# Performance work log

Measured on AMD Instinct MI355X. Metric: run time of the kernel, lower is better.

## Reference

```python
import jax, jax.numpy as jnp
import numpy as np

NF, B, C, H, W = 5, 8, 64, 128, 128

def setup_inputs() -> dict:
    key = jax.random.key(0)
    k1, k2, k3, k4, k5 = jax.random.split(key, 5)
    return {
        "inp": jax.random.normal(k1, (NF, B, C, H, W), dtype=jnp.float32),
        "origin_w": jax.random.normal(k2, (C, NF * C), dtype=jnp.float32) * 0.05,
        "origin_b": jax.random.normal(k3, (C,), dtype=jnp.float32) * 0.05,
        "out_w": jax.random.normal(k4, (1, 2 * C), dtype=jnp.float32) * 0.05,
        "out_b": jax.random.normal(k5, (1,), dtype=jnp.float32) * 0.05,
    }

def reference(inp, origin_w, origin_b, out_w, out_b):
    nf, b, c, h, w = inp.shape
    # concat frames along channel dim: [b, nf*c, h, w]
    x = jnp.transpose(inp, (1, 0, 2, 3, 4)).reshape(b, nf * c, h, w)
    # 1x1 conv -> origin query, viewed as [b, c, 1, h*w]
    origin = jnp.einsum('ok,bkhw->bohw', origin_w, x) + origin_b[None, :, None, None]
    origin = origin.reshape(b, c, 1, h * w)
    last = inp[-1]  # [b, c, h, w]
    # difference basis: [b, c, nf-1, h*w]
    basis = jnp.stack([last - inp[i] for i in range(nf - 1)], axis=2).reshape(b, c, nf - 1, h * w)
    # L2 normalize over the spatial (last) dim, torch F.normalize semantics (eps=1e-12)
    norm = jnp.sqrt(jnp.sum(basis * basis, axis=-1, keepdims=True))
    basis1 = basis / jnp.maximum(norm, 1e-12)
    # tiny-MN batched matmuls: [b,c,1,hw] x [b,c,hw,nf-1] -> [b,c,1,nf-1]
    score = jnp.einsum('bcik,bcjk->bcij', origin, basis1)
    # [b,c,1,nf-1] x [b,c,nf-1,hw] -> [b,c,1,hw]; original views back as (b,c,w,h)
    out = jnp.einsum('bcij,bcjk->bcik', score, basis1).reshape(b, c, w, h)
    cat = jnp.concatenate([out, last], axis=1)  # [b, 2c, h, w]
    y = jnp.einsum('ok,bkhw->bohw', out_w, cat) + out_b[None, :, None, None]
    return y
```

## Files before the change

### kernel.cpp

```cpp
#include <hip/hip_runtime.h>
#include <math.h>

#define NF 5
#define NB 8
#define NC 64
#define HW 16384
#define NK 320
#define FSTRIDE (NB*NC*HW)

#define EN_FLOATS    (NB*NC*8)

__global__ void k0_wp(const float* __restrict__ W, float* __restrict__ Wp,
                      float* __restrict__ EN){
    const int blk = blockIdx.x, tid = threadIdx.x;
    if (blk == 80){
        float4 z = make_float4(0.f,0.f,0.f,0.f);
#pragma unroll
        for (int j=0; j<4; ++j)
            reinterpret_cast<float4*>(EN)[tid*4 + j] = z;
        return;
    }
    int idx = blk*256 + tid;
    int c = idx / NK;
    int k = idx - c*NK;
    Wp[((c>>2)*NK + k)*4 + (c&3)] = W[idx];
}

__device__ __forceinline__ float redsum64(float v){
#pragma unroll
    for (int m = 1; m < 64; m <<= 1) v += __shfl_xor(v, m, 64);
    return v;
}

__global__ __launch_bounds__(256, 8) void k1_fused(
    const float* __restrict__ inp, const float* __restrict__ Wp,
    const float* __restrict__ bias, float* __restrict__ EN)
{
    const int tid = threadIdx.x;
    const int l   = tid & 63;
    const int wv  = __builtin_amdgcn_readfirstlane(tid >> 6);
    const int blk = blockIdx.x;
    const int xcd  = blk & 7;
    const int slot = blk >> 3;
    const int cgrp = slot & 3;
    const int g    = xcd*64 + (slot >> 2);
    const int b    = g >> 6;
    const int s0   = (g & 63) << 8;
    const int c0   = (cgrp << 4) + (wv << 2);
    const int sl   = __builtin_amdgcn_readfirstlane(c0 >> 2);

    float4 a0,a1,a2,a3;
    {
        float4 bv = *reinterpret_cast<const float4*>(bias + c0);
        a0 = make_float4(bv.x,bv.x,bv.x,bv.x);
        a1 = make_float4(bv.y,bv.y,bv.y,bv.y);
        a2 = make_float4(bv.z,bv.z,bv.z,bv.z);
        a3 = make_float4(bv.w,bv.w,bv.w,bv.w);
    }

    const float* wsl = Wp + (size_t)sl * (NK*4);

#define FMA4(A, WS) \
    A.x = fmaf(WS, xv.x, A.x); A.y = fmaf(WS, xv.y, A.y); \
    A.z = fmaf(WS, xv.z, A.z); A.w = fmaf(WS, xv.w, A.w);

#pragma unroll 1
    for (int f=0; f<NF; ++f){
        const float* xp = inp + (size_t)(f*NB + b)*NC*HW + s0 + (l << 2);
        const float* wf = wsl + f*256;
#pragma unroll 8
        for (int k=0; k<64; ++k){
            float4 xv = *reinterpret_cast<const float4*>(xp);
            xp += HW;
            float4 w  = *reinterpret_cast<const float4*>(wf + (k << 2));
            FMA4(a0, w.x) FMA4(a1, w.y) FMA4(a2, w.z) FMA4(a3, w.w)
        }
    }
#undef FMA4

#define PHASEB(CC, ACC) { \
    const float* cb = inp + ((size_t)b*NC + (c0+(CC)))*HW + s0 + (l << 2); \
    float4 x4 = *reinterpret_cast<const float4*>(cb + (size_t)4*FSTRIDE); \
    float ev[4], nv[4]; \
    _Pragma("unroll") \
    for (int i=0; i<4; ++i){ \
        float4 xi = *reinterpret_cast<const float4*>(cb + (size_t)i*FSTRIDE); \
        float dx = x4.x - xi.x, dy = x4.y - xi.y; \
        float dz = x4.z - xi.z, dw = x4.w - xi.w; \
        nv[i] = fmaf(dx,dx, fmaf(dy,dy, fmaf(dz,dz, dw*dw))); \
        ev[i] = fmaf((ACC).x,dx, fmaf((ACC).y,dy, fmaf((ACC).z,dz, (ACC).w*dw))); \
    } \
    _Pragma("unroll") \
    for (int i=0; i<4; ++i){ ev[i] = redsum64(ev[i]); nv[i] = redsum64(nv[i]); } \
    if (l == 0){ \
        float* p = EN + ((size_t)b*NC + c0 + (CC))*8; \
        atomicAdd(p+0, ev[0]); atomicAdd(p+1, ev[1]); \
        atomicAdd(p+2, ev[2]); atomicAdd(p+3, ev[3]); \
        atomicAdd(p+4, nv[0]); atomicAdd(p+5, nv[1]); \
        atomicAdd(p+6, nv[2]); atomicAdd(p+7, nv[3]); \
    } }

    PHASEB(0, a0) PHASEB(1, a1) PHASEB(2, a2) PHASEB(3, a3)
#undef PHASEB
}

__global__ __launch_bounds__(512) void k3_out(const float* __restrict__ inp,
        const float* __restrict__ EN, const float* __restrict__ out_w,
        const float* __restrict__ out_b, float* __restrict__ y)
{
    __shared__ float  Al[NK];
    __shared__ float4 P[512];
    const int tid = threadIdx.x;
    const int b   = blockIdx.x >> 6;
    const int s0  = (blockIdx.x & 63) << 8;
    const int sg  = tid & 63;
    const int rg  = __builtin_amdgcn_readfirstlane(tid >> 6);

    if (tid < 64){
        const int c = tid;
        const float* e = EN + ((size_t)b*NC + c)*8;
        float w1 = out_w[c], w2 = out_w[NC + c];
        float csum = 0.f;
#pragma unroll
        for (int i=0; i<4; ++i){
            float nc = fmaxf(sqrtf(e[4+i]), 1e-12f);
            float coef = e[i] / (nc*nc);
            Al[i*NC + c] = -w1*coef;
            csum += coef;
        }
        Al[4*NC + c] = w1*csum + w2;
    }
    __syncthreads();

    float4 acc = make_float4(0.f, 0.f, 0.f, 0.f);
    const int rbase = rg*40;
#pragma unroll 8
    for (int j=0; j<40; ++j){
        int r = rbase + j;
        const float* p = inp + (size_t)(((r>>6)*NB + b)*NC + (r&63))*HW + s0 + (sg<<2);
        float  w  = Al[r];
        float4 xv = *reinterpret_cast<const float4*>(p);
        acc.x = fmaf(w, xv.x, acc.x); acc.y = fmaf(w, xv.y, acc.y);
        acc.z = fmaf(w, xv.z, acc.z); acc.w = fmaf(w, xv.w, acc.w);
    }
    P[tid] = acc;
    __syncthreads();
    if (tid < 64){
        float4 r0 = P[tid];
        float vx = r0.x, vy = r0.y, vz = r0.z, vw = r0.w;
#pragma unroll
        for (int gg=1; gg<8; ++gg){
            float4 q = P[tid + (gg<<6)];
            vx += q.x; vy += q.y; vz += q.z; vw += q.w;
        }
        float bb = out_b[0];
        float4 o = make_float4(vx+bb, vy+bb, vz+bb, vw+bb);
        *reinterpret_cast<float4*>(y + (size_t)b*HW + s0 + (tid<<2)) = o;
    }
}

extern "C" void kernel_launch(void* const* d_in, const int* in_sizes, int n_in,
                              void* d_out, int out_size, void* d_ws, size_t ws_size,
                              hipStream_t stream)
{
    const float* inp      = (const float*)d_in[0];
    const float* origin_w = (const float*)d_in[1];
    const float* origin_b = (const float*)d_in[2];
    const float* out_w    = (const float*)d_in[3];
    const float* out_b    = (const float*)d_in[4];
    float* y  = (float*)d_out;
    float* ws = (float*)d_ws;

    float* EN = ws;
    float* Wp = ws + EN_FLOATS;

    k0_wp   <<<81,   256, 0, stream>>>(origin_w, Wp, EN);
    k1_fused<<<2048, 256, 0, stream>>>(inp, Wp, origin_b, EN);
    k3_out  <<<512,  512, 0, stream>>>(inp, EN, out_w, out_b, y);
}
```

Measured before the change: 353.5 us.

## Stage input rows through double-buffered LDS and split output reduction via atomics

The projection kernel now gives each block 1024 spatial positions for 16 output channels. Input rows are staged through a double-buffered shared-memory tile, so every wave reuses the same staged x data across its 4 channels and 4 spatial sub-tiles, with 16 float4 accumulators per thread. The grid drops from 2048 to 512 blocks with occupancy bound 2, trading fewer global re-reads of the input for more registers and lower parallelism. The output kernel splits its 320-row reduction across 8 separate blocks that atomically add into y, which k0 now zeroes, removing the in-block LDS reduction at the cost of float atomics and order-dependent rounding.

```diff
diff --git a/kernel.cpp b/kernel.cpp
--- a/kernel.cpp
+++ b/kernel.cpp
@@ -11,8 +11,15 @@
 #define EN_FLOATS    (NB*NC*8)
 
 __global__ void k0_wp(const float* __restrict__ W, float* __restrict__ Wp,
-                      float* __restrict__ EN){
+                      float* __restrict__ EN, float* __restrict__ y){
     const int blk = blockIdx.x, tid = threadIdx.x;
+    if (blk >= 81){
+        int i = (blk - 81)*256 + tid;
+        float4 z = make_float4(0.f,0.f,0.f,0.f);
+        reinterpret_cast<float4*>(y)[i*2]     = z;
+        reinterpret_cast<float4*>(y)[i*2 + 1] = z;
+        return;
+    }
     if (blk == 80){
         float4 z = make_float4(0.f,0.f,0.f,0.f);
 #pragma unroll
@@ -32,89 +39,143 @@
     return v;
 }
 
-__global__ __launch_bounds__(256, 8) void k1_fused(
+__global__ __launch_bounds__(256, 2) void k1_fused(
     const float* __restrict__ inp, const float* __restrict__ Wp,
     const float* __restrict__ bias, float* __restrict__ EN)
 {
+    __shared__ float S[2*8*1024];
+
     const int tid = threadIdx.x;
     const int l   = tid & 63;
     const int wv  = __builtin_amdgcn_readfirstlane(tid >> 6);
     const int blk = blockIdx.x;
     const int xcd  = blk & 7;
     const int slot = blk >> 3;
+    const int grp  = xcd*16 + (slot >> 2);
     const int cgrp = slot & 3;
-    const int g    = xcd*64 + (slot >> 2);
-    const int b    = g >> 6;
-    const int s0   = (g & 63) << 8;
-    const int c0   = (cgrp << 4) + (wv << 2);
-    const int sl   = __builtin_amdgcn_readfirstlane(c0 >> 2);
-
-    float4 a0,a1,a2,a3;
+    const int b    = grp >> 4;
+    const int s0   = (grp & 15) << 10;
+    const int cf   = (cgrp << 4) + (wv << 2);
+    const int sl   = __builtin_amdgcn_readfirstlane(cgrp*4 + wv);
+
+    float4 a00,a01,a02,a03, a10,a11,a12,a13, a20,a21,a22,a23, a30,a31,a32,a33;
     {
-        float4 bv = *reinterpret_cast<const float4*>(bias + c0);
-        a0 = make_float4(bv.x,bv.x,bv.x,bv.x);
-        a1 = make_float4(bv.y,bv.y,bv.y,bv.y);
-        a2 = make_float4(bv.z,bv.z,bv.z,bv.z);
-        a3 = make_float4(bv.w,bv.w,bv.w,bv.w);
-    }
-
-    const float* wsl = Wp + (size_t)sl * (NK*4);
-
-#define FMA4(A, WS) \
-    A.x = fmaf(WS, xv.x, A.x); A.y = fmaf(WS, xv.y, A.y); \
-    A.z = fmaf(WS, xv.z, A.z); A.w = fmaf(WS, xv.w, A.w);
+        float4 bv = *reinterpret_cast<const float4*>(bias + cf);
+        a00=a01=a02=a03 = make_float4(bv.x,bv.x,bv.x,bv.x);
+        a10=a11=a12=a13 = make_float4(bv.y,bv.y,bv.y,bv.y);
+        a20=a21=a22=a23 = make_float4(bv.z,bv.z,bv.z,bv.z);
+        a30=a31=a32=a33 = make_float4(bv.w,bv.w,bv.w,bv.w);
+    }
+
+    const float* Wk = Wp + (size_t)sl*(NK*4);
+
+#define ROWP(K) (inp + ((size_t)(((K)>>6)*NB + b)*NC + ((K)&63))*HW + s0 + (tid<<2))
+
+    float4 r0,r1,r2,r3,r4,r5,r6,r7;
+#define STAGE_LOAD(KT) { int K0 = (KT)*8; \
+    r0 = *reinterpret_cast<const float4*>(ROWP(K0+0)); \
+    r1 = *reinterpret_cast<const float4*>(ROWP(K0+1)); \
+    r2 = *reinterpret_cast<const float4*>(ROWP(K0+2)); \
+    r3 = *reinterpret_cast<const float4*>(ROWP(K0+3)); \
+    r4 = *reinterpret_cast<const float4*>(ROWP(K0+4)); \
+    r5 = *reinterpret_cast<const float4*>(ROWP(K0+5)); \
+    r6 = *reinterpret_cast<const float4*>(ROWP(K0+6)); \
+    r7 = *reinterpret_cast<const float4*>(ROWP(K0+7)); }
+
+#define STAGE_WRITE(BUF) { float* d = S + (BUF)*8192 + (tid<<2); \
+    *reinterpret_cast<float4*>(d + 0*1024) = r0; \
+    *reinterpret_cast<float4*>(d + 1*1024) = r1; \
+    *reinterpret_cast<float4*>(d + 2*1024) = r2; \
+    *reinterpret_cast<float4*>(d + 3*1024) = r3; \
+    *reinterpret_cast<float4*>(d + 4*1024) = r4; \
+    *reinterpret_cast<float4*>(d + 5*1024) = r5; \
+    *reinterpret_cast<float4*>(d + 6*1024) = r6; \
+    *reinterpret_cast<float4*>(d + 7*1024) = r7; }
+
+#define FMA4(A, WS, XV) \
+    A.x = fmaf(WS, XV.x, A.x); A.y = fmaf(WS, XV.y, A.y); \
+    A.z = fmaf(WS, XV.z, A.z); A.w = fmaf(WS, XV.w, A.w);
+
+    STAGE_LOAD(0)
+    STAGE_WRITE(0)
 
 #pragma unroll 1
-    for (int f=0; f<NF; ++f){
-        const float* xp = inp + (size_t)(f*NB + b)*NC*HW + s0 + (l << 2);
-        const float* wf = wsl + f*256;
-#pragma unroll 8
-        for (int k=0; k<64; ++k){
-            float4 xv = *reinterpret_cast<const float4*>(xp);
-            xp += HW;
-            float4 w  = *reinterpret_cast<const float4*>(wf + (k << 2));
-            FMA4(a0, w.x) FMA4(a1, w.y) FMA4(a2, w.z) FMA4(a3, w.w)
+    for (int kt=0; kt<40; ++kt){
+        __syncthreads();
+        if (kt < 39) STAGE_LOAD(kt+1)
+        const float* X = S + (kt&1)*8192 + (l<<2);
+#pragma unroll 2
+        for (int k=0; k<8; ++k){
+            float4 w  = *reinterpret_cast<const float4*>(Wk + ((kt*8+k)<<2));
+            float4 x0 = *reinterpret_cast<const float4*>(X + k*1024);
+            float4 x1 = *reinterpret_cast<const float4*>(X + k*1024 + 256);
+            float4 x2 = *reinterpret_cast<const float4*>(X + k*1024 + 512);
+            float4 x3 = *reinterpret_cast<const float4*>(X + k*1024 + 768);
+            FMA4(a00,w.x,x0) FMA4(a01,w.x,x1) FMA4(a02,w.x,x2) FMA4(a03,w.x,x3)
+            FMA4(a10,w.y,x0) FMA4(a11,w.y,x1) FMA4(a12,w.y,x2) FMA4(a13,w.y,x3)
+            FMA4(a20,w.z,x0) FMA4(a21,w.z,x1) FMA4(a22,w.z,x2) FMA4(a23,w.z,x3)
+            FMA4(a30,w.w,x0) FMA4(a31,w.w,x1) FMA4(a32,w.w,x2) FMA4(a33,w.w,x3)
         }
+        if (kt < 39) STAGE_WRITE((kt+1)&1)
     }
 #undef FMA4
-
-#define PHASEB(CC, ACC) { \
-    const float* cb = inp + ((size_t)b*NC + (c0+(CC)))*HW + s0 + (l << 2); \
-    float4 x4 = *reinterpret_cast<const float4*>(cb + (size_t)4*FSTRIDE); \
-    float ev[4], nv[4]; \
+#undef STAGE_LOAD
+#undef STAGE_WRITE
+#undef ROWP
+
+#define PHASEB(CH, A0, A1, A2, A3) { \
+    const float* p4 = inp + ((size_t)(4*NB + b)*NC + (cf+(CH)))*HW + s0 + (l<<2); \
+    float4 x40 = *reinterpret_cast<const float4*>(p4); \
+    float4 x41 = *reinterpret_cast<const float4*>(p4 + 256); \
+    float4 x42 = *reinterpret_cast<const float4*>(p4 + 512); \
+    float4 x43 = *reinterpret_cast<const float4*>(p4 + 768); \
     _Pragma("unroll") \
     for (int i=0; i<4; ++i){ \
-        float4 xi = *reinterpret_cast<const float4*>(cb + (size_t)i*FSTRIDE); \
-        float dx = x4.x - xi.x, dy = x4.y - xi.y; \
-        float dz = x4.z - xi.z, dw = x4.w - xi.w; \
-        nv[i] = fmaf(dx,dx, fmaf(dy,dy, fmaf(dz,dz, dw*dw))); \
-        ev[i] = fmaf((ACC).x,dx, fmaf((ACC).y,dy, fmaf((ACC).z,dz, (ACC).w*dw))); \
-    } \
-    _Pragma("unroll") \
-    for (int i=0; i<4; ++i){ ev[i] = redsum64(ev[i]); nv[i] = redsum64(nv[i]); } \
-    if (l == 0){ \
-        float* p = EN + ((size_t)b*NC + c0 + (CC))*8; \
-        atomicAdd(p+0, ev[0]); atomicAdd(p+1, ev[1]); \
-        atomicAdd(p+2, ev[2]); atomicAdd(p+3, ev[3]); \
-        atomicAdd(p+4, nv[0]); atomicAdd(p+5, nv[1]); \
-        atomicAdd(p+6, nv[2]); atomicAdd(p+7, nv[3]); \
+        const float* pi = inp + ((size_t)(i*NB + b)*NC + (cf+(CH)))*HW + s0 + (l<<2); \
+        float4 xi0 = *reinterpret_cast<const float4*>(pi); \
+        float4 xi1 = *reinterpret_cast<const float4*>(pi + 256); \
+        float4 xi2 = *reinterpret_cast<const float4*>(pi + 512); \
+        float4 xi3 = *reinterpret_cast<const float4*>(pi + 768); \
+        float e = 0.f, n = 0.f; \
+        float dx,dy,dz,dw; \
+        dx=x40.x-xi0.x; dy=x40.y-xi0.y; dz=x40.z-xi0.z; dw=x40.w-xi0.w; \
+        n = fmaf(dx,dx, fmaf(dy,dy, fmaf(dz,dz, fmaf(dw,dw, n)))); \
+        e = fmaf(A0.x,dx, fmaf(A0.y,dy, fmaf(A0.z,dz, fmaf(A0.w,dw, e)))); \
+        dx=x41.x-xi1.x; dy=x41.y-xi1.y; dz=x41.z-xi1.z; dw=x41.w-xi1.w; \
+        n = fmaf(dx,dx, fmaf(dy,dy, fmaf(dz,dz, fmaf(dw,dw, n)))); \
+        e = fmaf(A1.x,dx, fmaf(A1.y,dy, fmaf(A1.z,dz, fmaf(A1.w,dw, e)))); \
+        dx=x42.x-xi2.x; dy=x42.y-xi2.y; dz=x42.z-xi2.z; dw=x42.w-xi2.w; \
+        n = fmaf(dx,dx, fmaf(dy,dy, fmaf(dz,dz, fmaf(dw,dw, n)))); \
+        e = fmaf(A2.x,dx, fmaf(A2.y,dy, fmaf(A2.z,dz, fmaf(A2.w,dw, e)))); \
+        dx=x43.x-xi3.x; dy=x43.y-xi3.y; dz=x43.z-xi3.z; dw=x43.w-xi3.w; \
+        n = fmaf(dx,dx, fmaf(dy,dy, fmaf(dz,dz, fmaf(dw,dw, n)))); \
+        e = fmaf(A3.x,dx, fmaf(A3.y,dy, fmaf(A3.z,dz, fmaf(A3.w,dw, e)))); \
+        e = redsum64(e); n = redsum64(n); \
+        if (l == 0){ \
+            float* p = EN + ((size_t)b*NC + cf + (CH))*8; \
+            atomicAdd(p + i,     e); \
+            atomicAdd(p + 4 + i, n); \
+        } \
     } }
 
-    PHASEB(0, a0) PHASEB(1, a1) PHASEB(2, a2) PHASEB(3, a3)
+    PHASEB(0, a00,a01,a02,a03)
+    PHASEB(1, a10,a11,a12,a13)
+    PHASEB(2, a20,a21,a22,a23)
+    PHASEB(3, a30,a31,a32,a33)
 #undef PHASEB
 }
 
-__global__ __launch_bounds__(512) void k3_out(const float* __restrict__ inp,
+__global__ __launch_bounds__(256, 4) void k3_out(const float* __restrict__ inp,
         const float* __restrict__ EN, const float* __restrict__ out_w,
         const float* __restrict__ out_b, float* __restrict__ y)
 {
-    __shared__ float  Al[NK];
-    __shared__ float4 P[512];
+    __shared__ float Al[NK];
     const int tid = threadIdx.x;
-    const int b   = blockIdx.x >> 6;
-    const int s0  = (blockIdx.x & 63) << 8;
-    const int sg  = tid & 63;
-    const int rg  = __builtin_amdgcn_readfirstlane(tid >> 6);
+    const int blk = blockIdx.x;
+    const int b   = blk >> 7;
+    const int ch  = (blk >> 3) & 15;
+    const int rg  = blk & 7;
+    const int s0  = ch << 10;
 
     if (tid < 64){
         const int c = tid;
@@ -132,31 +193,25 @@
     }
     __syncthreads();
 
-    float4 acc = make_float4(0.f, 0.f, 0.f, 0.f);
+    float4 acc;
+    if (rg == 0){ float bb = out_b[0]; acc = make_float4(bb,bb,bb,bb); }
+    else        { acc = make_float4(0.f,0.f,0.f,0.f); }
+
     const int rbase = rg*40;
 #pragma unroll 8
     for (int j=0; j<40; ++j){
         int r = rbase + j;
-        const float* p = inp + (size_t)(((r>>6)*NB + b)*NC + (r&63))*HW + s0 + (sg<<2);
+        const float* p = inp + (size_t)(((r>>6)*NB + b)*NC + (r&63))*HW + s0 + (tid<<2);
         float  w  = Al[r];
         float4 xv = *reinterpret_cast<const float4*>(p);
         acc.x = fmaf(w, xv.x, acc.x); acc.y = fmaf(w, xv.y, acc.y);
         acc.z = fmaf(w, xv.z, acc.z); acc.w = fmaf(w, xv.w, acc.w);
     }
-    P[tid] = acc;
-    __syncthreads();
-    if (tid < 64){
-        float4 r0 = P[tid];
-        float vx = r0.x, vy = r0.y, vz = r0.z, vw = r0.w;
-#pragma unroll
-        for (int gg=1; gg<8; ++gg){
-            float4 q = P[tid + (gg<<6)];
-            vx += q.x; vy += q.y; vz += q.z; vw += q.w;
-        }
-        float bb = out_b[0];
-        float4 o = make_float4(vx+bb, vy+bb, vz+bb, vw+bb);
-        *reinterpret_cast<float4*>(y + (size_t)b*HW + s0 + (tid<<2)) = o;
-    }
+    float* yp = y + (size_t)b*HW + s0 + (tid<<2);
+    atomicAdd(yp+0, acc.x);
+    atomicAdd(yp+1, acc.y);
+    atomicAdd(yp+2, acc.z);
+    atomicAdd(yp+3, acc.w);
 }
 
 extern "C" void kernel_launch(void* const* d_in, const int* in_sizes, int n_in,
@@ -174,7 +229,7 @@
     float* EN = ws;
     float* Wp = ws + EN_FLOATS;
 
-    k0_wp   <<<81,   256, 0, stream>>>(origin_w, Wp, EN);
-    k1_fused<<<2048, 256, 0, stream>>>(inp, Wp, origin_b, EN);
-    k3_out  <<<512,  512, 0, stream>>>(inp, EN, out_w, out_b, y);
-}
+    k0_wp   <<<145,  256, 0, stream>>>(origin_w, Wp, EN, y);
+    k1_fused<<<512,  256, 0, stream>>>(inp, Wp, origin_b, EN);
+    k3_out  <<<1024, 256, 0, stream>>>(inp, EN, out_w, out_b, y);
+}
```

After: 303.8 us. -14.0%, faster.

## Stage conv inputs in double-buffered LDS tiles and split output reduction via atomics

Applied to the files above, without the earlier changes.

The 1x1 conv kernel now stages 8-row input slices of a 512-wide spatial window in double-buffered shared memory, loading ahead through registers. Each wave computes 4 channels over 512 positions, which halves the block count and reads weights directly instead of through a pre-packed copy. The output kernel splits the 320-row reduction across 16 blocks that atomically add into a pre-zeroed y, replacing the in-block LDS reduction. The goal is more input reuse per load and better latency hiding. The cost is extra synchronisation, lower occupancy, and float atomics on the output, which make the summation order nondeterministic.

```diff
diff --git a/kernel.cpp b/kernel.cpp
--- a/kernel.cpp
+++ b/kernel.cpp
@@ -6,25 +6,10 @@
 #define NC 64
 #define HW 16384
 #define NK 320
-#define FSTRIDE (NB*NC*HW)
-
-#define EN_FLOATS    (NB*NC*8)
-
-__global__ void k0_wp(const float* __restrict__ W, float* __restrict__ Wp,
-                      float* __restrict__ EN){
-    const int blk = blockIdx.x, tid = threadIdx.x;
-    if (blk == 80){
-        float4 z = make_float4(0.f,0.f,0.f,0.f);
-#pragma unroll
-        for (int j=0; j<4; ++j)
-            reinterpret_cast<float4*>(EN)[tid*4 + j] = z;
-        return;
-    }
-    int idx = blk*256 + tid;
-    int c = idx / NK;
-    int k = idx - c*NK;
-    Wp[((c>>2)*NK + k)*4 + (c&3)] = W[idx];
-}
+#define EN_FLOATS (NB*NC*8)
+
+#define WIN 512
+#define NT  40
 
 __device__ __forceinline__ float redsum64(float v){
 #pragma unroll
@@ -32,89 +17,145 @@
     return v;
 }
 
-__global__ __launch_bounds__(256, 8) void k1_fused(
-    const float* __restrict__ inp, const float* __restrict__ Wp,
+__global__ void k0z(float* __restrict__ EN, float* __restrict__ y){
+    const int blk = blockIdx.x, tid = threadIdx.x;
+    float4 z = make_float4(0.f,0.f,0.f,0.f);
+    if (blk == 0){
+#pragma unroll
+        for (int j=0; j<4; ++j)
+            reinterpret_cast<float4*>(EN)[tid*4 + j] = z;
+    } else {
+        int i = (blk - 1)*512 + tid*2;
+        reinterpret_cast<float4*>(y)[i]     = z;
+        reinterpret_cast<float4*>(y)[i + 1] = z;
+    }
+}
+
+__global__ __launch_bounds__(256, 4) void k1_fused(
+    const float* __restrict__ inp, const float* __restrict__ Wg,
     const float* __restrict__ bias, float* __restrict__ EN)
 {
+    __shared__ float S[2*8*WIN];
+
     const int tid = threadIdx.x;
-    const int l   = tid & 63;
-    const int wv  = __builtin_amdgcn_readfirstlane(tid >> 6);
-    const int blk = blockIdx.x;
+    const int l    = tid & 63;
+    const int wv   = __builtin_amdgcn_readfirstlane(tid >> 6);
+    const int blk  = blockIdx.x;
     const int xcd  = blk & 7;
-    const int slot = blk >> 3;
-    const int cgrp = slot & 3;
-    const int g    = xcd*64 + (slot >> 2);
-    const int b    = g >> 6;
-    const int s0   = (g & 63) << 8;
-    const int c0   = (cgrp << 4) + (wv << 2);
-    const int sl   = __builtin_amdgcn_readfirstlane(c0 >> 2);
-
-    float4 a0,a1,a2,a3;
+    const int q    = blk >> 3;
+    const int cgrp = q & 3;
+    const int unit = xcd*32 + (q >> 2);
+    const int b    = unit >> 5;
+    const int sbase= (unit & 31) << 9;
+    const int cf   = (cgrp << 4) + (wv << 2);
+    const int hi   = tid >> 7;
+    const int col  = (tid & 127) << 2;
+
+    const float* w0r = Wg + (size_t)(cf+0)*NK;
+    const float* w1r = Wg + (size_t)(cf+1)*NK;
+    const float* w2r = Wg + (size_t)(cf+2)*NK;
+    const float* w3r = Wg + (size_t)(cf+3)*NK;
+
+    float4 c0p0,c0p1,c1p0,c1p1,c2p0,c2p1,c3p0,c3p1;
     {
-        float4 bv = *reinterpret_cast<const float4*>(bias + c0);
-        a0 = make_float4(bv.x,bv.x,bv.x,bv.x);
-        a1 = make_float4(bv.y,bv.y,bv.y,bv.y);
-        a2 = make_float4(bv.z,bv.z,bv.z,bv.z);
-        a3 = make_float4(bv.w,bv.w,bv.w,bv.w);
-    }
-
-    const float* wsl = Wp + (size_t)sl * (NK*4);
-
-#define FMA4(A, WS) \
-    A.x = fmaf(WS, xv.x, A.x); A.y = fmaf(WS, xv.y, A.y); \
-    A.z = fmaf(WS, xv.z, A.z); A.w = fmaf(WS, xv.w, A.w);
-
-#pragma unroll 1
-    for (int f=0; f<NF; ++f){
-        const float* xp = inp + (size_t)(f*NB + b)*NC*HW + s0 + (l << 2);
-        const float* wf = wsl + f*256;
-#pragma unroll 8
-        for (int k=0; k<64; ++k){
-            float4 xv = *reinterpret_cast<const float4*>(xp);
-            xp += HW;
-            float4 w  = *reinterpret_cast<const float4*>(wf + (k << 2));
-            FMA4(a0, w.x) FMA4(a1, w.y) FMA4(a2, w.z) FMA4(a3, w.w)
+        float4 bv = *reinterpret_cast<const float4*>(bias + cf);
+        c0p0=c0p1 = make_float4(bv.x,bv.x,bv.x,bv.x);
+        c1p0=c1p1 = make_float4(bv.y,bv.y,bv.y,bv.y);
+        c2p0=c2p1 = make_float4(bv.z,bv.z,bv.z,bv.z);
+        c3p0=c3p1 = make_float4(bv.w,bv.w,bv.w,bv.w);
+    }
+
+#define XADDR(K) (inp + ((size_t)((((K)>>6))*NB + b)*NC + ((K)&63))*HW + sbase + col)
+#define LOADSET(R0,R1,R2,R3, KT) { \
+    R0 = *reinterpret_cast<const float4*>(XADDR((KT)*8 + 0 + hi)); \
+    R1 = *reinterpret_cast<const float4*>(XADDR((KT)*8 + 2 + hi)); \
+    R2 = *reinterpret_cast<const float4*>(XADDR((KT)*8 + 4 + hi)); \
+    R3 = *reinterpret_cast<const float4*>(XADDR((KT)*8 + 6 + hi)); }
+#define WRITESET(R0,R1,R2,R3, BUF) { \
+    float* d = S + (BUF)*(8*WIN) + hi*WIN + col; \
+    *reinterpret_cast<float4*>(d + 0*WIN) = R0; \
+    *reinterpret_cast<float4*>(d + 2*WIN) = R1; \
+    *reinterpret_cast<float4*>(d + 4*WIN) = R2; \
+    *reinterpret_cast<float4*>(d + 6*WIN) = R3; }
+#define FMA4(A, WS, XV) \
+    A.x = fmaf(WS, XV.x, A.x); A.y = fmaf(WS, XV.y, A.y); \
+    A.z = fmaf(WS, XV.z, A.z); A.w = fmaf(WS, XV.w, A.w);
+
+    float4 rA0,rA1,rA2,rA3, rB0,rB1,rB2,rB3;
+    LOADSET(rA0,rA1,rA2,rA3, 0)
+    LOADSET(rB0,rB1,rB2,rB3, 1)
+    WRITESET(rA0,rA1,rA2,rA3, 0)
+    LOADSET(rA0,rA1,rA2,rA3, 2)
+    __syncthreads();
+
+#pragma unroll 2
+    for (int kt=0; kt<NT; ++kt){
+        if (kt & 1){
+            if (kt < NT-1) WRITESET(rA0,rA1,rA2,rA3, (kt+1)&1)
+            if (kt < NT-3) LOADSET (rA0,rA1,rA2,rA3, kt+3)
+        } else {
+            if (kt < NT-1) WRITESET(rB0,rB1,rB2,rB3, (kt+1)&1)
+            if (kt < NT-3) LOADSET (rB0,rB1,rB2,rB3, kt+3)
         }
+        const float* X = S + (kt&1)*(8*WIN) + (l<<2);
+        const int K0 = kt*8;
+#pragma unroll 4
+        for (int k=0; k<8; ++k){
+            float w0 = w0r[K0+k], w1 = w1r[K0+k];
+            float w2 = w2r[K0+k], w3 = w3r[K0+k];
+            float4 x0 = *reinterpret_cast<const float4*>(X + k*WIN);
+            float4 x1 = *reinterpret_cast<const float4*>(X + k*WIN + 256);
+            FMA4(c0p0,w0,x0) FMA4(c0p1,w0,x1)
+            FMA4(c1p0,w1,x0) FMA4(c1p1,w1,x1)
+            FMA4(c2p0,w2,x0) FMA4(c2p1,w2,x1)
+            FMA4(c3p0,w3,x0) FMA4(c3p1,w3,x1)
+        }
+        __syncthreads();
     }
 #undef FMA4
-
-#define PHASEB(CC, ACC) { \
-    const float* cb = inp + ((size_t)b*NC + (c0+(CC)))*HW + s0 + (l << 2); \
-    float4 x4 = *reinterpret_cast<const float4*>(cb + (size_t)4*FSTRIDE); \
-    float ev[4], nv[4]; \
+#undef LOADSET
+#undef WRITESET
+#undef XADDR
+
+#define PHB(J, A0, A1) { \
+    const float* p4 = inp + ((size_t)(4*NB + b)*NC + (cf+(J)))*HW + sbase + (l<<2); \
+    float4 x40 = *reinterpret_cast<const float4*>(p4); \
+    float4 x41 = *reinterpret_cast<const float4*>(p4 + 256); \
     _Pragma("unroll") \
     for (int i=0; i<4; ++i){ \
-        float4 xi = *reinterpret_cast<const float4*>(cb + (size_t)i*FSTRIDE); \
-        float dx = x4.x - xi.x, dy = x4.y - xi.y; \
-        float dz = x4.z - xi.z, dw = x4.w - xi.w; \
-        nv[i] = fmaf(dx,dx, fmaf(dy,dy, fmaf(dz,dz, dw*dw))); \
-        ev[i] = fmaf((ACC).x,dx, fmaf((ACC).y,dy, fmaf((ACC).z,dz, (ACC).w*dw))); \
-    } \
-    _Pragma("unroll") \
-    for (int i=0; i<4; ++i){ ev[i] = redsum64(ev[i]); nv[i] = redsum64(nv[i]); } \
-    if (l == 0){ \
-        float* p = EN + ((size_t)b*NC + c0 + (CC))*8; \
-        atomicAdd(p+0, ev[0]); atomicAdd(p+1, ev[1]); \
-        atomicAdd(p+2, ev[2]); atomicAdd(p+3, ev[3]); \
-        atomicAdd(p+4, nv[0]); atomicAdd(p+5, nv[1]); \
-        atomicAdd(p+6, nv[2]); atomicAdd(p+7, nv[3]); \
+        const float* pi = inp + ((size_t)((i)*NB + b)*NC + (cf+(J)))*HW + sbase + (l<<2); \
+        float4 xi0 = *reinterpret_cast<const float4*>(pi); \
+        float4 xi1 = *reinterpret_cast<const float4*>(pi + 256); \
+        float dx,dy,dz,dw,e,n; \
+        dx=x40.x-xi0.x; dy=x40.y-xi0.y; dz=x40.z-xi0.z; dw=x40.w-xi0.w; \
+        n = fmaf(dx,dx, fmaf(dy,dy, fmaf(dz,dz, dw*dw))); \
+        e = fmaf((A0).x,dx, fmaf((A0).y,dy, fmaf((A0).z,dz, (A0).w*dw))); \
+        dx=x41.x-xi1.x; dy=x41.y-xi1.y; dz=x41.z-xi1.z; dw=x41.w-xi1.w; \
+        n = fmaf(dx,dx, fmaf(dy,dy, fmaf(dz,dz, fmaf(dw,dw, n)))); \
+        e = fmaf((A1).x,dx, fmaf((A1).y,dy, fmaf((A1).z,dz, fmaf((A1).w,dw, e)))); \
+        e = redsum64(e); n = redsum64(n); \
+        if (l == 0){ \
+            float* p = EN + ((size_t)b*NC + cf + (J))*8; \
+            atomicAdd(p + i, e); atomicAdd(p + 4 + i, n); \
+        } \
     } }
 
-    PHASEB(0, a0) PHASEB(1, a1) PHASEB(2, a2) PHASEB(3, a3)
-#undef PHASEB
-}
-
-__global__ __launch_bounds__(512) void k3_out(const float* __restrict__ inp,
+    PHB(0, c0p0, c0p1) PHB(1, c1p0, c1p1)
+    PHB(2, c2p0, c2p1) PHB(3, c3p0, c3p1)
+#undef PHB
+}
+
+__global__ __launch_bounds__(256, 8) void k3_out(const float* __restrict__ inp,
         const float* __restrict__ EN, const float* __restrict__ out_w,
         const float* __restrict__ out_b, float* __restrict__ y)
 {
-    __shared__ float  Al[NK];
-    __shared__ float4 P[512];
+    __shared__ float Al[NK];
     const int tid = threadIdx.x;
-    const int b   = blockIdx.x >> 6;
-    const int s0  = (blockIdx.x & 63) << 8;
-    const int sg  = tid & 63;
-    const int rg  = __builtin_amdgcn_readfirstlane(tid >> 6);
+    const int blk = blockIdx.x;
+    const int b   = blk >> 8;
+    const int ck  = (blk >> 4) & 15;
+    const int rg  = blk & 15;
+    const int s0  = ck << 10;
 
     if (tid < 64){
         const int c = tid;
@@ -132,31 +173,25 @@
     }
     __syncthreads();
 
-    float4 acc = make_float4(0.f, 0.f, 0.f, 0.f);
-    const int rbase = rg*40;
-#pragma unroll 8
-    for (int j=0; j<40; ++j){
+    float4 acc;
+    if (rg == 0){ float bb = out_b[0]; acc = make_float4(bb,bb,bb,bb); }
+    else        { acc = make_float4(0.f,0.f,0.f,0.f); }
+
+    const int rbase = rg*20;
+#pragma unroll 4
+    for (int j=0; j<20; ++j){
         int r = rbase + j;
-        const float* p = inp + (size_t)(((r>>6)*NB + b)*NC + (r&63))*HW + s0 + (sg<<2);
+        const float* p = inp + ((size_t)((r>>6)*NB + b)*NC + (r&63))*HW + s0 + (tid<<2);
         float  w  = Al[r];
         float4 xv = *reinterpret_cast<const float4*>(p);
         acc.x = fmaf(w, xv.x, acc.x); acc.y = fmaf(w, xv.y, acc.y);
         acc.z = fmaf(w, xv.z, acc.z); acc.w = fmaf(w, xv.w, acc.w);
     }
-    P[tid] = acc;
-    __syncthreads();
-    if (tid < 64){
-        float4 r0 = P[tid];
-        float vx = r0.x, vy = r0.y, vz = r0.z, vw = r0.w;
-#pragma unroll
-        for (int gg=1; gg<8; ++gg){
-            float4 q = P[tid + (gg<<6)];
-            vx += q.x; vy += q.y; vz += q.z; vw += q.w;
-        }
-        float bb = out_b[0];
-        float4 o = make_float4(vx+bb, vy+bb, vz+bb, vw+bb);
-        *reinterpret_cast<float4*>(y + (size_t)b*HW + s0 + (tid<<2)) = o;
-    }
+    float* yp = y + (size_t)b*HW + s0 + (tid<<2);
+    atomicAdd(yp+0, acc.x);
+    atomicAdd(yp+1, acc.y);
+    atomicAdd(yp+2, acc.z);
+    atomicAdd(yp+3, acc.w);
 }
 
 extern "C" void kernel_launch(void* const* d_in, const int* in_sizes, int n_in,
@@ -169,12 +204,9 @@
     const float* out_w    = (const float*)d_in[3];
     const float* out_b    = (const float*)d_in[4];
     float* y  = (float*)d_out;
-    float* ws = (float*)d_ws;
-
-    float* EN = ws;
-    float* Wp = ws + EN_FLOATS;
-
-    k0_wp   <<<81,   256, 0, stream>>>(origin_w, Wp, EN);
-    k1_fused<<<2048, 256, 0, stream>>>(inp, Wp, origin_b, EN);
-    k3_out  <<<512,  512, 0, stream>>>(inp, EN, out_w, out_b, y);
-}
+    float* EN = (float*)d_ws;
+
+    k0z     <<<65,   256, 0, stream>>>(EN, y);
+    k1_fused<<<1024, 256, 0, stream>>>(inp, origin_w, origin_b, EN);
+    k3_out  <<<2048, 256, 0, stream>>>(inp, EN, out_w, out_b, y);
+}
```

Result: faster. 307.6 us (-13.0%).

## Stage input tiles in LDS with double buffering and widen per-wave channel tile

Applied to the files above, without the earlier changes.

The 1x1-conv kernel now loads 8-row input slabs cooperatively into a double-buffered shared-memory tile and reuses each slab across 8 output channels per wave, instead of 4 channels per wave reading input straight from global memory. Blocks halve to 1024 and occupancy drops to 4 per CU in exchange for more reuse per load. The weight-prepack kernel is removed in favour of reading the raw weights and a memset for the accumulator. The output kernel is reshaped to 256-thread blocks over 128-pixel tiles. The aim is to cut redundant global input traffic, which costs more registers, LDS and barriers.

```diff
diff --git a/kernel.cpp b/kernel.cpp
--- a/kernel.cpp
+++ b/kernel.cpp
@@ -6,25 +6,10 @@
 #define NC 64
 #define HW 16384
 #define NK 320
-#define FSTRIDE (NB*NC*HW)
+#define EN_FLOATS (NB*NC*8)
 
-#define EN_FLOATS    (NB*NC*8)
-
-__global__ void k0_wp(const float* __restrict__ W, float* __restrict__ Wp,
-                      float* __restrict__ EN){
-    const int blk = blockIdx.x, tid = threadIdx.x;
-    if (blk == 80){
-        float4 z = make_float4(0.f,0.f,0.f,0.f);
-#pragma unroll
-        for (int j=0; j<4; ++j)
-            reinterpret_cast<float4*>(EN)[tid*4 + j] = z;
-        return;
-    }
-    int idx = blk*256 + tid;
-    int c = idx / NK;
-    int k = idx - c*NK;
-    Wp[((c>>2)*NK + k)*4 + (c&3)] = W[idx];
-}
+#define WIN1 256
+#define NT  40
 
 __device__ __forceinline__ float redsum64(float v){
 #pragma unroll
@@ -32,89 +17,120 @@
     return v;
 }
 
-__global__ __launch_bounds__(256, 8) void k1_fused(
-    const float* __restrict__ inp, const float* __restrict__ Wp,
+__global__ __launch_bounds__(256, 4) void k1_fused(
+    const float* __restrict__ inp, const float* __restrict__ Wg,
     const float* __restrict__ bias, float* __restrict__ EN)
 {
+    __shared__ float S[2*8*WIN1];
+
     const int tid = threadIdx.x;
-    const int l   = tid & 63;
-    const int wv  = __builtin_amdgcn_readfirstlane(tid >> 6);
-    const int blk = blockIdx.x;
+    const int l    = tid & 63;
+    const int wv   = __builtin_amdgcn_readfirstlane(tid >> 6);
+    const int blk  = blockIdx.x;
     const int xcd  = blk & 7;
-    const int slot = blk >> 3;
-    const int cgrp = slot & 3;
-    const int g    = xcd*64 + (slot >> 2);
-    const int b    = g >> 6;
-    const int s0   = (g & 63) << 8;
-    const int c0   = (cgrp << 4) + (wv << 2);
-    const int sl   = __builtin_amdgcn_readfirstlane(c0 >> 2);
+    const int q    = blk >> 3;
+    const int cgrp = q & 1;
+    const int unit = xcd*64 + (q >> 1);
+    const int b    = unit >> 6;
+    const int s0   = (unit & 63) << 8;
+    const int cf   = (cgrp << 5) + (wv << 3);
+    const int srow = tid >> 5;
+    const int scol = (tid & 31) << 2;
 
-    float4 a0,a1,a2,a3;
+    float4 A[8];
     {
-        float4 bv = *reinterpret_cast<const float4*>(bias + c0);
-        a0 = make_float4(bv.x,bv.x,bv.x,bv.x);
-        a1 = make_float4(bv.y,bv.y,bv.y,bv.y);
-        a2 = make_float4(bv.z,bv.z,bv.z,bv.z);
-        a3 = make_float4(bv.w,bv.w,bv.w,bv.w);
+        float4 b0 = *reinterpret_cast<const float4*>(bias + cf);
+        float4 b1 = *reinterpret_cast<const float4*>(bias + cf + 4);
+        A[0] = make_float4(b0.x,b0.x,b0.x,b0.x);
+        A[1] = make_float4(b0.y,b0.y,b0.y,b0.y);
+        A[2] = make_float4(b0.z,b0.z,b0.z,b0.z);
+        A[3] = make_float4(b0.w,b0.w,b0.w,b0.w);
+        A[4] = make_float4(b1.x,b1.x,b1.x,b1.x);
+        A[5] = make_float4(b1.y,b1.y,b1.y,b1.y);
+        A[6] = make_float4(b1.z,b1.z,b1.z,b1.z);
+        A[7] = make_float4(b1.w,b1.w,b1.w,b1.w);
     }
 
-    const float* wsl = Wp + (size_t)sl * (NK*4);
+    const float* wbase = Wg + (size_t)cf*NK;
 
-#define FMA4(A, WS) \
-    A.x = fmaf(WS, xv.x, A.x); A.y = fmaf(WS, xv.y, A.y); \
-    A.z = fmaf(WS, xv.z, A.z); A.w = fmaf(WS, xv.w, A.w);
+#define XROW(K) (inp + ((size_t)(((K)>>6)*NB + b)*NC + ((K)&63))*HW + s0 + scol)
+#define LOADSET(R0,R1, KT) { const float* _p = XROW((KT)*8 + srow); \
+    R0 = *reinterpret_cast<const float4*>(_p); \
+    R1 = *reinterpret_cast<const float4*>(_p + 128); }
+#define WRITESET(R0,R1, BUF) { float* _d = S + (BUF)*(8*WIN1) + srow*WIN1 + scol; \
+    *reinterpret_cast<float4*>(_d)       = R0; \
+    *reinterpret_cast<float4*>(_d + 128) = R1; }
 
-#pragma unroll 1
-    for (int f=0; f<NF; ++f){
-        const float* xp = inp + (size_t)(f*NB + b)*NC*HW + s0 + (l << 2);
-        const float* wf = wsl + f*256;
-#pragma unroll 8
-        for (int k=0; k<64; ++k){
-            float4 xv = *reinterpret_cast<const float4*>(xp);
-            xp += HW;
-            float4 w  = *reinterpret_cast<const float4*>(wf + (k << 2));
-            FMA4(a0, w.x) FMA4(a1, w.y) FMA4(a2, w.z) FMA4(a3, w.w)
+    float4 rA0,rA1, rB0,rB1;
+    LOADSET(rA0,rA1, 0)
+    LOADSET(rB0,rB1, 1)
+    WRITESET(rA0,rA1, 0)
+    LOADSET(rA0,rA1, 2)
+    __syncthreads();
+
+#pragma unroll 2
+    for (int kt=0; kt<NT; ++kt){
+        if (kt & 1){
+            if (kt < NT-1) WRITESET(rA0,rA1, (kt+1)&1)
+            if (kt < NT-3) LOADSET (rA0,rA1, kt+3)
+        } else {
+            if (kt < NT-1) WRITESET(rB0,rB1, (kt+1)&1)
+            if (kt < NT-3) LOADSET (rB0,rB1, kt+3)
+        }
+        const float* X  = S + (kt&1)*(8*WIN1) + (l<<2);
+        const float* wt = wbase + kt*8;
+#pragma unroll
+        for (int k=0; k<8; ++k){
+            float4 xv = *reinterpret_cast<const float4*>(X + k*WIN1);
+#pragma unroll
+            for (int j=0; j<8; ++j){
+                float w = wt[(size_t)j*NK + k];
+                A[j].x = fmaf(w, xv.x, A[j].x);
+                A[j].y = fmaf(w, xv.y, A[j].y);
+                A[j].z = fmaf(w, xv.z, A[j].z);
+                A[j].w = fmaf(w, xv.w, A[j].w);
+            }
+        }
+        __syncthreads();
+    }
+#undef LOADSET
+#undef WRITESET
+#undef XROW
+
+#pragma unroll
+    for (int j=0; j<8; ++j){
+        const float* p4 = inp + ((size_t)(4*NB + b)*NC + (cf+j))*HW + s0 + (l<<2);
+        float4 x4 = *reinterpret_cast<const float4*>(p4);
+#pragma unroll
+        for (int i=0; i<4; ++i){
+            const float* pi = inp + ((size_t)(i*NB + b)*NC + (cf+j))*HW + s0 + (l<<2);
+            float4 xi = *reinterpret_cast<const float4*>(pi);
+            float dx = x4.x - xi.x, dy = x4.y - xi.y;
+            float dz = x4.z - xi.z, dw = x4.w - xi.w;
+            float n = fmaf(dx,dx, fmaf(dy,dy, fmaf(dz,dz, dw*dw)));
+            float e = fmaf(A[j].x,dx, fmaf(A[j].y,dy, fmaf(A[j].z,dz, A[j].w*dw)));
+            e = redsum64(e); n = redsum64(n);
+            if (l == 0){
+                float* p = EN + ((size_t)b*NC + cf + j)*8;
+                atomicAdd(p + i,     e);
+                atomicAdd(p + 4 + i, n);
+            }
         }
     }
-#undef FMA4
-
-#define PHASEB(CC, ACC) { \
-    const float* cb = inp + ((size_t)b*NC + (c0+(CC)))*HW + s0 + (l << 2); \
-    float4 x4 = *reinterpret_cast<const float4*>(cb + (size_t)4*FSTRIDE); \
-    float ev[4], nv[4]; \
-    _Pragma("unroll") \
-    for (int i=0; i<4; ++i){ \
-        float4 xi = *reinterpret_cast<const float4*>(cb + (size_t)i*FSTRIDE); \
-        float dx = x4.x - xi.x, dy = x4.y - xi.y; \
-        float dz = x4.z - xi.z, dw = x4.w - xi.w; \
-        nv[i] = fmaf(dx,dx, fmaf(dy,dy, fmaf(dz,dz, dw*dw))); \
-        ev[i] = fmaf((ACC).x,dx, fmaf((ACC).y,dy, fmaf((ACC).z,dz, (ACC).w*dw))); \
-    } \
-    _Pragma("unroll") \
-    for (int i=0; i<4; ++i){ ev[i] = redsum64(ev[i]); nv[i] = redsum64(nv[i]); } \
-    if (l == 0){ \
-        float* p = EN + ((size_t)b*NC + c0 + (CC))*8; \
-        atomicAdd(p+0, ev[0]); atomicAdd(p+1, ev[1]); \
-        atomicAdd(p+2, ev[2]); atomicAdd(p+3, ev[3]); \
-        atomicAdd(p+4, nv[0]); atomicAdd(p+5, nv[1]); \
-        atomicAdd(p+6, nv[2]); atomicAdd(p+7, nv[3]); \
-    } }
-
-    PHASEB(0, a0) PHASEB(1, a1) PHASEB(2, a2) PHASEB(3, a3)
-#undef PHASEB
 }
 
-__global__ __launch_bounds__(512) void k3_out(const float* __restrict__ inp,
+__global__ __launch_bounds__(256, 8) void k3_out(const float* __restrict__ inp,
         const float* __restrict__ EN, const float* __restrict__ out_w,
         const float* __restrict__ out_b, float* __restrict__ y)
 {
     __shared__ float  Al[NK];
-    __shared__ float4 P[512];
+    __shared__ float4 P[256];
     const int tid = threadIdx.x;
-    const int b   = blockIdx.x >> 6;
-    const int s0  = (blockIdx.x & 63) << 8;
-    const int sg  = tid & 63;
-    const int rg  = __builtin_amdgcn_readfirstlane(tid >> 6);
+    const int blk = blockIdx.x;
+    const int b   = blk >> 7;
+    const int s0  = (blk & 127) << 7;
+    const int sg  = tid & 31;
+    const int rg  = tid >> 5;
 
     if (tid < 64){
         const int c = tid;
@@ -132,12 +148,12 @@
     }
     __syncthreads();
 
-    float4 acc = make_float4(0.f, 0.f, 0.f, 0.f);
+    float4 acc = make_float4(0.f,0.f,0.f,0.f);
     const int rbase = rg*40;
 #pragma unroll 8
     for (int j=0; j<40; ++j){
         int r = rbase + j;
-        const float* p = inp + (size_t)(((r>>6)*NB + b)*NC + (r&63))*HW + s0 + (sg<<2);
+        const float* p = inp + ((size_t)((r>>6)*NB + b)*NC + (r&63))*HW + s0 + (sg<<2);
         float  w  = Al[r];
         float4 xv = *reinterpret_cast<const float4*>(p);
         acc.x = fmaf(w, xv.x, acc.x); acc.y = fmaf(w, xv.y, acc.y);
@@ -145,12 +161,12 @@
     }
     P[tid] = acc;
     __syncthreads();
-    if (tid < 64){
+    if (tid < 32){
         float4 r0 = P[tid];
         float vx = r0.x, vy = r0.y, vz = r0.z, vw = r0.w;
 #pragma unroll
-        for (int gg=1; gg<8; ++gg){
-            float4 q = P[tid + (gg<<6)];
+        for (int g=1; g<8; ++g){
+            float4 q = P[tid + (g<<5)];
             vx += q.x; vy += q.y; vz += q.z; vw += q.w;
         }
         float bb = out_b[0];
@@ -169,12 +185,9 @@
     const float* out_w    = (const float*)d_in[3];
     const float* out_b    = (const float*)d_in[4];
     float* y  = (float*)d_out;
-    float* ws = (float*)d_ws;
+    float* EN = (float*)d_ws;
 
-    float* EN = ws;
-    float* Wp = ws + EN_FLOATS;
-
-    k0_wp   <<<81,   256, 0, stream>>>(origin_w, Wp, EN);
-    k1_fused<<<2048, 256, 0, stream>>>(inp, Wp, origin_b, EN);
-    k3_out  <<<512,  512, 0, stream>>>(inp, EN, out_w, out_b, y);
+    hipMemsetAsync(EN, 0, EN_FLOATS*sizeof(float), stream);
+    k1_fused<<<1024, 256, 0, stream>>>(inp, origin_w, origin_b, EN);
+    k3_out  <<<1024, 256, 0, stream>>>(inp, EN, out_w, out_b, y);
 }
```

Result: faster. 308.7 us (-12.7%).
